# Kernel tuning notes

Measured on AMD Instinct MI355X. Metric: run time of the kernel, lower is better.

## Reference

```python
import math
import jax, jax.numpy as jnp
import numpy as np

R = 4  # upsample_factor
C_FEAT = 22
FEAT_SLICES = {4: (0, 9), 6: (9, 22)}
SH_SLICES = {0: (0, 1), 2: (1, 6)}
AGG_PATHS = [(4, 0, 4), (4, 2, 4), (4, 2, 6), (6, 0, 6), (6, 2, 4), (6, 2, 6)]
TP_PATHS = [(4, 4, 4), (4, 4, 6), (4, 6, 4), (4, 6, 6), (6, 4, 4), (6, 4, 6), (6, 6, 4), (6, 6, 6)]
AGG_NPATH = {4: 3, 6: 3}
TP_NPATH = {4: 4, 6: 4}


def _cg(j1, m1, j2, m2, j3, m3):
    # Condon-Shortley Clebsch-Gordan <j1 m1 j2 m2 | j3 m3> (Racah formula)
    if m1 + m2 != m3:
        return 0.0
    f = math.factorial
    pre = (2 * j3 + 1) * f(j1 + j2 - j3) * f(j1 - j2 + j3) * f(-j1 + j2 + j3) / f(j1 + j2 + j3 + 1)
    pre *= f(j1 + m1) * f(j1 - m1) * f(j2 + m2) * f(j2 - m2) * f(j3 + m3) * f(j3 - m3)
    kmin = max(0, j2 - j3 - m1, j1 - j3 + m2)
    kmax = min(j1 + j2 - j3, j1 - m1, j2 + m2)
    s = 0.0
    for k in range(kmin, kmax + 1):
        s += (-1) ** k / (f(k) * f(j1 + j2 - j3 - k) * f(j1 - m1 - k) * f(j2 + m2 - k) * f(j3 - j2 + m1 + k) * f(j3 - j1 - m2 + k))
    return math.sqrt(pre) * s


def _q(l):
    # change of basis real SH -> complex SH (rows: real m, cols: complex m), with (-i)^l phase
    q = np.zeros((2 * l + 1, 2 * l + 1), dtype=np.complex128)
    q[l, l] = 1.0
    s2 = 1.0 / math.sqrt(2.0)
    for m in range(1, l + 1):
        q[l + m, l + m] = (-1) ** m * s2
        q[l + m, l - m] = s2
        q[l - m, l - m] = 1j * s2
        q[l - m, l + m] = -1j * (-1) ** m * s2
    return ((-1j) ** l) * q


def _w3j_real(l1, l2, l3):
    # Wigner 3j tensor in the real spherical-harmonic basis (invariant, unit Frobenius norm)
    w = np.zeros((2 * l1 + 1, 2 * l2 + 1, 2 * l3 + 1))
    for m1 in range(-l1, l1 + 1):
        for m2 in range(-l2, l2 + 1):
            m3 = -(m1 + m2)
            if abs(m3) <= l3:
                w[l1 + m1, l2 + m2, l3 + m3] = ((-1) ** (l1 - l2 - m3)) / math.sqrt(2 * l3 + 1) * _cg(l1, m1, l2, m2, l3, -m3)
    c = np.einsum('ai,bj,ck,ijk->abc', _q(l1), _q(l2), _q(l3), w.astype(np.complex128))
    return np.real(c).astype(np.float32)  # l1+l2+l3 even -> real


CG = {p: jnp.asarray(_w3j_real(*p)) for p in set(AGG_PATHS) | set(TP_PATHS)}


def _sh_kernel():
    # even-l real SH (integral normalization) at the 4 fixed 2x2 kernel directions
    s = 1.0 / math.sqrt(2.0)
    dirs = np.array([[-s, -s, 0.0], [s, -s, 0.0], [-s, s, 0.0], [s, s, 0.0]])
    x, y, z = dirs[:, 0], dirs[:, 1], dirs[:, 2]
    c2 = math.sqrt(15.0 / math.pi)
    sh = np.stack([
        np.full(4, 0.5 / math.sqrt(math.pi)),      # l=0
        0.5 * c2 * x * y,                           # l=2, m=-2
        0.5 * c2 * y * z,                           # l=2, m=-1
        0.25 * math.sqrt(5.0 / math.pi) * (3 * z ** 2 - 1.0),  # l=2, m=0
        0.5 * c2 * x * z,                           # l=2, m=1
        0.25 * c2 * (x ** 2 - y ** 2),              # l=2, m=2
    ], axis=1)
    return jnp.asarray(sh.astype(np.float32))  # (4, 6)


SH_KERNEL = _sh_kernel()


def setup_inputs() -> dict:
    key = jax.random.key(0)
    k1, k2, k3, k4 = jax.random.split(key, 4)
    H = W = 256
    return {
        'f4': jax.random.normal(k1, (H * W, 9), dtype=jnp.float32),
        'f6': jax.random.normal(k2, (H * W, 13), dtype=jnp.float32),
        'img_h': H,
        'img_w': W,
        'w_agg': jax.random.normal(k3, (6,), dtype=jnp.float32) * 0.1,
        'w_tp': jax.random.normal(k4, (8,), dtype=jnp.float32) * 0.1,
    }


def reference(f4, f6, img_h, img_w, w_agg, w_tp):
    H, W = int(img_h), int(img_w)
    Hr, Wr = H * R, W * R
    N = Hr * Wr
    # 1. nearest-neighbour upsample of concatenated irreps (H,W,22) -> (Hr,Wr,22)
    feat = jnp.concatenate([f4, f6], axis=-1).reshape(H, W, C_FEAT)
    feat_hr = jnp.repeat(jnp.repeat(feat, R, axis=0), R, axis=1)
    # 2. gather 2x2 patches with replicate padding (matches unfold k ordering (dh,dw))
    pad = jnp.pad(feat_hr, ((0, 1), (0, 1), (0, 0)), mode='edge')
    patches = jnp.stack([pad[dh:dh + Hr, dw:dw + Wr] for dh, dw in ((0, 0), (0, 1), (1, 0), (1, 1))], axis=2)
    patches = patches.reshape(N, 4, C_FEAT)  # (N,4,22)
    # tp_aggregate(neighbour, sh) summed over the 4 neighbours -> context (N,22)
    context = jnp.zeros((N, C_FEAT), dtype=feat.dtype)
    for i, (l1, l2, l3) in enumerate(AGG_PATHS):
        a0, a1 = FEAT_SLICES[l1]
        b0, b1 = SH_SLICES[l2]
        c0, c1 = FEAT_SLICES[l3]
        alpha = math.sqrt((2 * l3 + 1) / AGG_NPATH[l3])
        contrib = jnp.einsum('nka,kb,abc->nc', patches[:, :, a0:a1], SH_KERNEL[:, b0:b1], CG[(l1, l2, l3)])
        context = context.at[:, c0:c1].add((w_agg[i] * alpha) * contrib)
    # 3. tp(feat_self, context)
    feat_flat = feat_hr.reshape(N, C_FEAT)
    out = jnp.zeros((N, C_FEAT), dtype=feat.dtype)
    for i, (l1, l2, l3) in enumerate(TP_PATHS):
        a0, a1 = FEAT_SLICES[l1]
        b0, b1 = FEAT_SLICES[l2]
        c0, c1 = FEAT_SLICES[l3]
        alpha = math.sqrt((2 * l3 + 1) / TP_NPATH[l3])
        contrib = jnp.einsum('na,nb,abc->nc', feat_flat[:, a0:a1], context[:, b0:b1], CG[(l1, l2, l3)])
        out = out.at[:, c0:c1].add((w_tp[i] * alpha) * contrib)
    # 4. residual from the NN-upsampled features
    f4_out = out[:, :9] + feat_flat[:, :9]
    f6_out = out[:, 9:] + feat_flat[:, 9:]
    return f4_out, f6_out, (Hr, Wr)
```

## Files before the change

kernel.cpp:

```cpp
#include <hip/hip_runtime.h>
#include <hip/hip_bf16.h>
#include <math.h>

typedef __attribute__((ext_vector_type(8))) short short8;
typedef __attribute__((ext_vector_type(4))) float f32x4;
typedef __attribute__((ext_vector_type(2))) float f32x2;

__constant__ float c_fact[20] = {
    1.0f, 1.0f, 2.0f, 6.0f, 24.0f, 120.0f, 720.0f, 5040.0f, 40320.0f, 362880.0f,
    3628800.0f, 39916800.0f, 479001600.0f, 6227020800.0f, 87178291200.0f,
    1307674368000.0f, 20922789888000.0f, 355687428096000.0f,
    6402373705728000.0f, 121645100408832000.0f};
__constant__ float c_invf[20] = {
    1.0f, 1.0f, 0.5f, 0.16666666666666666f, 0.041666666666666664f,
    0.008333333333333333f, 0.001388888888888889f, 1.984126984126984e-4f,
    2.48015873015873e-5f, 2.755731922398589e-6f, 2.755731922398589e-7f,
    2.505210838544172e-8f, 2.08767569878681e-9f, 1.6059043836821613e-10f,
    1.1470745597729725e-11f, 7.647163731819816e-13f, 4.779477332387385e-14f,
    2.8114572543455206e-15f, 1.5619206968586225e-16f, 8.22063524662433e-18f};

__device__ float cgd(int j1, int m1, int j2, int m2, int j3, int m3) {
  if (m1 + m2 != m3) return 0.0f;
  float pre = (float)(2 * j3 + 1) * c_fact[j1 + j2 - j3] * c_fact[j1 - j2 + j3] *
              c_fact[-j1 + j2 + j3] * c_invf[j1 + j2 + j3 + 1];
  pre *= c_fact[j1 + m1] * c_fact[j1 - m1] * c_fact[j2 + m2] * c_fact[j2 - m2] *
         c_fact[j3 + m3] * c_fact[j3 - m3];
  int kmin = max(0, max(j2 - j3 - m1, j1 - j3 + m2));
  int kmax = min(j1 + j2 - j3, min(j1 - m1, j2 + m2));
  float s = 0.0f;
  for (int k = kmin; k <= kmax; ++k) {
    float d = c_invf[k] * c_invf[j1 + j2 - j3 - k] * c_invf[j1 - m1 - k] *
              c_invf[j2 + m2 - k] * c_invf[j3 - j2 + m1 + k] * c_invf[j3 - j1 - m2 + k];
    s += ((k & 1) ? -d : d);
  }
  return sqrtf(pre) * s;
}

__device__ float wstd(int l1, int l2, int l3, int i, int j, int k) {
  int m1 = i - l1, m2 = j - l2, m3 = k - l3;
  if (m1 + m2 + m3 != 0) return 0.0f;
  int e = l1 - l2 - m3;
  float sgn = (e & 1) ? -1.0f : 1.0f;
  return sgn * (1.0f / sqrtf((float)(2 * l3 + 1))) * cgd(l1, m1, l2, m2, l3, -m3);
}

__device__ int qrow(int l, int a, int idx[2], float vr[2], float vi[2]) {
  const float s2 = 0.70710678118654752440f;
  int m = a - l;
  if (m == 0) { idx[0] = l; vr[0] = 1.0f; vi[0] = 0.0f; return 1; }
  if (m > 0) {
    idx[0] = l + m; vr[0] = (m & 1) ? -s2 : s2; vi[0] = 0.0f;
    idx[1] = l - m; vr[1] = s2;                 vi[1] = 0.0f;
    return 2;
  }
  int mm = -m;
  idx[0] = l - mm; vr[0] = 0.0f; vi[0] = s2;
  idx[1] = l + mm; vr[1] = 0.0f; vi[1] = (mm & 1) ? s2 : -s2;
  return 2;
}

__device__ float w3j_real(int l1, int l2, int l3, int a, int b, int c) {
  int i1[2], i2[2], i3[2];
  float r1[2], s1[2], r2[2], s2v[2], r3[2], s3[2];
  int n1 = qrow(l1, a, i1, r1, s1);
  int n2 = qrow(l2, b, i2, r2, s2v);
  int n3 = qrow(l3, c, i3, r3, s3);
  float re = 0.0f;
  for (int x = 0; x < n1; ++x)
    for (int y = 0; y < n2; ++y)
      for (int z = 0; z < n3; ++z) {
        float w = wstd(l1, l2, l3, i1[x], i2[y], i3[z]);
        if (w == 0.0f) continue;
        float pr = r1[x] * r2[y] - s1[x] * s2v[y];
        float pi = r1[x] * s2v[y] + s1[x] * r2[y];
        float qr = pr * r3[z] - pi * s3[z];
        re += qr * w;
      }
  int L = l1 + l2 + l3;
  return ((L & 3) == 0) ? re : -re;
}

__device__ float sh_val(int k, int col) {
  const float PI_ = 3.14159265358979323846f;
  float sgn = (k == 0 || k == 3) ? 1.0f : -1.0f;
  if (col == 0) return 0.5f / sqrtf(PI_);
  if (col == 1) return sgn * 0.25f * sqrtf(15.0f / PI_);
  if (col == 3) return -0.25f * sqrtf(5.0f / PI_);
  return 0.0f;
}

__device__ __forceinline__ unsigned short bf16u(float x) {
  __hip_bfloat16 h = __float2bfloat16(x);
  return __builtin_bit_cast(unsigned short, h);
}
__device__ __forceinline__ float b2f(unsigned short u) {
  unsigned int v = ((unsigned int)u) << 16;
  return __builtin_bit_cast(float, v);
}

__global__ void eq_setup(const float* __restrict__ w_agg, const float* __restrict__ w_tp,
                         const int* __restrict__ ph, const int* __restrict__ pw,
                         float* __restrict__ out, long long tail_off,
                         unsigned short* __restrict__ ws) {
  int gid = blockIdx.x * 256 + threadIdx.x;
  if (gid == 0) {
    out[tail_off]     = (float)(ph[0] * 4);
    out[tail_off + 1] = (float)(pw[0] * 4);
  }
  if (gid < 22528) {
    int a = gid >> 10;
    int rem = gid & 1023;
    int nt = rem >> 9;
    int l = (rem >> 3) & 63;
    int e = rem & 7;
    int b = ((l >> 4) << 3) + e;
    int c = nt * 16 + (l & 15);
    float v = 0.f;
    if (b < 22 && c < 22) {
      int l1 = (a < 9) ? 4 : 6, l2 = (b < 9) ? 4 : 6, l3 = (c < 9) ? 4 : 6;
      int a_ = (a < 9) ? a : a - 9, b_ = (b < 9) ? b : b - 9, c_ = (c < 9) ? c : c - 9;
      int idx = ((l1 == 6) ? 4 : 0) + ((l2 == 6) ? 2 : 0) + ((l3 == 6) ? 1 : 0);
      float alpha = sqrtf((float)(2 * l3 + 1) * 0.25f);
      v = w_tp[idx] * alpha * w3j_real(l1, l2, l3, a_, b_, c_);
    }
    int pk = __builtin_amdgcn_cvt_pk_fp8_f32(v, 0.f, 0, 0);
    ((unsigned char*)ws)[gid] = (unsigned char)(pk & 0xff);
  } else if (gid < 26624) {
    int s = gid - 22528;
    int km = s >> 10;
    int rem = s & 1023;
    int nt = rem >> 9;
    int l = (rem >> 3) & 63;
    int e = rem & 7;
    int a = ((l >> 4) << 3) + e;
    int c = nt * 16 + (l & 15);
    float v = 0.f;
    if (a < 22 && c < 22) {
      int l1 = (a < 9) ? 4 : 6, l3 = (c < 9) ? 4 : 6;
      int a_ = (a < 9) ? a : a - 9, c_ = (c < 9) ? c : c - 9;
      float acc = 0.0f;
      float alpha = sqrtf((float)(2 * l3 + 1) / 3.0f);
      if (l1 == l3) {
        int i = (l1 == 4) ? 0 : 3;
        acc += w_agg[i] * alpha * sh_val(km, 0) * w3j_real(l1, 0, l3, a_, 0, c_);
      }
      {
        int i = (l1 == 4) ? ((l3 == 4) ? 1 : 2) : ((l3 == 4) ? 4 : 5);
        float t = 0.0f;
        for (int bb = 0; bb < 5; ++bb) {
          float shv = sh_val(km, 1 + bb);
          if (shv != 0.0f) t += shv * w3j_real(l1, 2, l3, a_, bb, c_);
        }
        acc += w_agg[i] * alpha * t;
      }
      v = acc;
    }
    ws[11264 + s] = bf16u(v);
  }
}

__device__ __forceinline__ void load_lds16(const unsigned int* g, unsigned int* l) {
  __builtin_amdgcn_global_load_lds(
      (const __attribute__((address_space(1))) unsigned int*)g,
      (__attribute__((address_space(3))) unsigned int*)l, 16, 0, 0);
}

#define WAVE_LDS_FENCE() do { \
    asm volatile("s_waitcnt lgkmcnt(0)" ::: "memory"); \
    __builtin_amdgcn_sched_barrier(0); } while (0)

__global__ __launch_bounds__(512, 6) void eq_main(
    const float* __restrict__ f4, const float* __restrict__ f6,
    const int* __restrict__ ph, const int* __restrict__ pw,
    const unsigned short* __restrict__ ws, float* __restrict__ out) {
  const int H = ph[0], Wc = pw[0];
  const int bx = (Wc + 31) >> 5;
  const long long ntiles = (long long)bx * H;
  const int Wr = Wc << 2;
  const long long Npix = (long long)H * Wc * 16;
  float* out6 = out + Npix * 9;

  __shared__ __align__(16) unsigned short LDS[23040];

  const int tid = threadIdx.x;
  const int wv = tid >> 6;
  const int l = tid & 63;
  const long long t = blockIdx.x;
  if (t >= ntiles) return;

  const int y0 = (int)(t / bx);
  const int x0 = (int)(t - (long long)y0 * bx) << 5;
  const int cw0 = x0 + (wv << 2);
  const int SLOT = 11264 + wv * 1472;

  {
    const unsigned int* src = (const unsigned int*)ws;
    unsigned int* dst = (unsigned int*)LDS;
#pragma unroll
    for (int i = 0; i < 3; ++i) {
      int chunk = i * 8 + wv;
      if (chunk < 22) load_lds16(src + chunk * 256 + l * 4, dst + chunk * 256);
    }
  }

  short8 mb[8];
  {
    const unsigned short* msrc = ws + 11264;
#pragma unroll
    for (int i = 0; i < 8; ++i) mb[i] = *(const short8*)(msrc + i * 512 + l * 8);
  }

#pragma unroll
  for (int k = 0; k < 2; ++k) {
    int e = k * 64 + l;
    if (e < 110) {
      int px = e / 11, pr = e - px * 11;
      int dyR = px / 5, col = px - dyR * 5;
      int yy = min(y0 + dyR, H - 1);
      int xx = min(cw0 + col, Wc - 1);
      long long p = (long long)yy * Wc + xx;
      int ca = 2 * pr;
      float v0 = (ca < 9) ? f4[p * 9 + ca] : f6[p * 13 + ca - 9];
      float v1 = (ca + 1 < 9) ? f4[p * 9 + ca + 1] : f6[p * 13 + ca - 8];
      unsigned int pk = (unsigned int)bf16u(v0) | ((unsigned int)bf16u(v1) << 16);
      *(unsigned int*)&LDS[SLOT + px * 24 + ca] = pk;
    } else if (e < 120) {
      *(unsigned int*)&LDS[SLOT + (e - 110) * 24 + 22] = 0u;
    }
  }

  __syncthreads();

  const int l15 = l & 15;
  const int lg = l >> 4;
  const int q = l15 & 3;
  const int lcell = l15 >> 2;
  const int a0 = lg << 3;

  f32x4 c0 = {0.f, 0.f, 0.f, 0.f}, c1 = {0.f, 0.f, 0.f, 0.f};
#pragma unroll
  for (int km = 0; km < 4; ++km) {
    short8 av = (short8)0;
    if (a0 < 24) {
      int dy = (km >> 1) & (q >> 1);
      int dx = km & q & 1;
      av = *(const short8*)&LDS[SLOT + (dy * 5 + lcell + dx) * 24 + a0];
    }
    c0 = __builtin_amdgcn_mfma_f32_16x16x32_bf16(av, mb[2 * km], c0, 0, 0, 0);
    c1 = __builtin_amdgcn_mfma_f32_16x16x32_bf16(av, mb[2 * km + 1], c1, 0, 0, 0);
  }

  unsigned int fvp[11];
  {
    const unsigned int* fp = (const unsigned int*)&LDS[SLOT + lcell * 24];
#pragma unroll
    for (int j = 0; j < 11; ++j) fvp[j] = fp[j];
  }
  const float r4 = b2f(LDS[SLOT + lg * 24 + l15]);
  const float r6 = (l15 < 6) ? b2f(LDS[SLOT + lg * 24 + 16 + l15]) : 0.f;

  float* ctxf = (float*)&LDS[SLOT + 256];
#pragma unroll
  for (int r = 0; r < 4; ++r) {
    ctxf[l15 * 24 + (lg << 2) + r] = c0[r];
    int ch1 = 16 + (lg << 2) + r;
    if (ch1 < 22) ctxf[l15 * 24 + ch1] = c1[r];
  }
  if (lg == 0) { ctxf[l15 * 24 + 22] = 0.f; ctxf[l15 * 24 + 23] = 0.f; }
  WAVE_LDS_FENCE();

  f32x2 cv2[4];
  {
    f32x4 lo = {0.f, 0.f, 0.f, 0.f}, hi = {0.f, 0.f, 0.f, 0.f};
    if (a0 < 24) {
      lo = *(const f32x4*)(ctxf + l15 * 24 + a0);
      hi = *(const f32x4*)(ctxf + l15 * 24 + a0 + 4);
    }
    cv2[0][0] = lo[0]; cv2[0][1] = lo[1];
    cv2[1][0] = lo[2]; cv2[1][1] = lo[3];
    cv2[2][0] = hi[0]; cv2[2][1] = hi[1];
    cv2[3][0] = hi[2]; cv2[3][1] = hi[3];
  }
  WAVE_LDS_FENCE();

  f32x4 oE0 = {0.f, 0.f, 0.f, 0.f}, oE1 = {0.f, 0.f, 0.f, 0.f};
  f32x4 oO0 = {0.f, 0.f, 0.f, 0.f}, oO1 = {0.f, 0.f, 0.f, 0.f};
  const char* Wb = (const char*)LDS;
#pragma unroll
  for (int ap = 0; ap < 11; ++ap) {
    const float sE = __builtin_bit_cast(float, fvp[ap] << 16);
    const float sO = __builtin_bit_cast(float, fvp[ap] & 0xffff0000u);
    {
      const f32x2 s2 = {sE, sE};
      f32x2 p0 = cv2[0] * s2, p1 = cv2[1] * s2, p2 = cv2[2] * s2, p3 = cv2[3] * s2;
      int lo = __builtin_amdgcn_cvt_pk_fp8_f32(p0[0], p0[1], 0, 0);
      lo = __builtin_amdgcn_cvt_pk_fp8_f32(p1[0], p1[1], lo, 1);
      int hi = __builtin_amdgcn_cvt_pk_fp8_f32(p2[0], p2[1], 0, 0);
      hi = __builtin_amdgcn_cvt_pk_fp8_f32(p3[0], p3[1], hi, 1);
      long av = (long)(((unsigned long long)(unsigned int)hi << 32) | (unsigned int)lo);
      long w0 = *(const long*)(Wb + ap * 2048 + l * 8);
      long w1 = *(const long*)(Wb + ap * 2048 + 512 + l * 8);
      oE0 = __builtin_amdgcn_mfma_f32_16x16x32_fp8_fp8(av, w0, oE0, 0, 0, 0);
      oE1 = __builtin_amdgcn_mfma_f32_16x16x32_fp8_fp8(av, w1, oE1, 0, 0, 0);
    }
    {
      const f32x2 s2 = {sO, sO};
      f32x2 p0 = cv2[0] * s2, p1 = cv2[1] * s2, p2 = cv2[2] * s2, p3 = cv2[3] * s2;
      int lo = __builtin_amdgcn_cvt_pk_fp8_f32(p0[0], p0[1], 0, 0);
      lo = __builtin_amdgcn_cvt_pk_fp8_f32(p1[0], p1[1], lo, 1);
      int hi = __builtin_amdgcn_cvt_pk_fp8_f32(p2[0], p2[1], 0, 0);
      hi = __builtin_amdgcn_cvt_pk_fp8_f32(p3[0], p3[1], hi, 1);
      long av = (long)(((unsigned long long)(unsigned int)hi << 32) | (unsigned int)lo);
      long w0 = *(const long*)(Wb + ap * 2048 + 1024 + l * 8);
      long w1 = *(const long*)(Wb + ap * 2048 + 1536 + l * 8);
      oO0 = __builtin_amdgcn_mfma_f32_16x16x32_fp8_fp8(av, w0, oO0, 0, 0, 0);
      oO1 = __builtin_amdgcn_mfma_f32_16x16x32_fp8_fp8(av, w1, oO1, 0, 0, 0);
    }
  }

  float* px4 = (float*)&LDS[SLOT];
  float* px6 = px4 + 288;
#pragma unroll
  for (int r = 0; r < 4; ++r) {
    const float v  = oE0[r] + oO0[r] + r4;
    const float v1 = oE1[r] + oO1[r] + r6;
    const int qy = r >> 1;
    float* p4 = px4 + qy * 144;
    float* p6 = px6 + qy * 208;
    if (r & 1) {
      const int px = (lg << 2) + 3;
      if (l15 < 9) p4[px * 9 + l15] = v; else p6[px * 13 + l15 - 9] = v;
      if (l15 < 6) p6[px * 13 + 7 + l15] = v1;
    } else {
#pragma unroll
      for (int dx = 0; dx < 3; ++dx) {
        const int px = (lg << 2) + dx;
        if (l15 < 9) p4[px * 9 + l15] = v; else p6[px * 13 + l15 - 9] = v;
        if (l15 < 6) p6[px * 13 + 7 + l15] = v1;
      }
    }
  }
  WAVE_LDS_FENCE();

  const long long y4 = (long long)(y0 << 2);
  if (cw0 + 4 <= Wc) {
#pragma unroll
    for (int ry = 0; ry < 4; ++ry) {
      const int qy = (ry == 3) ? 1 : 0;
      float* o4p = out + ((y4 + ry) * Wr + (cw0 << 2)) * 9;
      float* o6p = out6 + ((y4 + ry) * Wr + (cw0 << 2)) * 13;
      if (l < 36) *(f32x4*)(o4p + (l << 2)) = *(const f32x4*)(px4 + qy * 144 + (l << 2));
      if (l < 52) *(f32x4*)(o6p + (l << 2)) = *(const f32x4*)(px6 + qy * 208 + (l << 2));
    }
  } else {
    const int px = l & 15;
    const int ry = l >> 4;
    const int qy = (ry == 3) ? 1 : 0;
    const int hrx = (cw0 << 2) + px;
    if (hrx < Wr) {
      const long long rowb = (y4 + ry) * Wr + hrx;
      float* o4 = out + rowb * 9;
      float* o6 = out6 + rowb * 13;
#pragma unroll
      for (int ch = 0; ch < 9; ++ch) o4[ch] = px4[qy * 144 + px * 9 + ch];
#pragma unroll
      for (int ch = 0; ch < 13; ++ch) o6[ch] = px6[qy * 208 + px * 13 + ch];
    }
  }
}

extern "C" void kernel_launch(void* const* d_in, const int* in_sizes, int n_in,
                              void* d_out, int out_size, void* d_ws, size_t ws_size,
                              hipStream_t stream) {
  const float* f4 = (const float*)d_in[0];
  const float* f6 = (const float*)d_in[1];
  const int* ph = (const int*)d_in[2];
  const int* pw = (const int*)d_in[3];
  const float* wagg = (const float*)d_in[4];
  const float* wtp = (const float*)d_in[5];
  float* out = (float*)d_out;
  unsigned short* wsu = (unsigned short*)d_ws;

  long long HW = (long long)in_sizes[0] / 9;
  long long tail = (long long)out_size - 2;

  eq_setup<<<104, 256, 0, stream>>>(wagg, wtp, ph, pw, out, tail, wsu);

  int S = (int)(sqrt((double)HW) + 0.5);
  long long nb;
  if ((long long)S * S == HW) {
    nb = (long long)((S + 31) / 32) * S;
  } else {
    nb = HW;
  }
  eq_main<<<(int)nb, 512, 0, stream>>>(f4, f6, ph, pw, wsu, out);
}
```

Before: 46.09 us.

## Interleave fp8 TP weights for 128-bit LDS loads and vectorize LDS traffic

Reorders the fp8 tensor-product weight table in the workspace so each lane's four 8-byte MFMA B operands sit next to each other, letting the inner loop fetch them with two 16-byte LDS reads instead of four 8-byte reads. The per-pixel feature read and the context write-back now use vector LDS accesses instead of scalar loops. The block-wide barrier after patch staging becomes a wave-local fence, and a block barrier is placed before the weight-consuming loop with a wave fence after it. This cuts LDS instruction count but depends on the new barrier placement still ordering the cooperative weight staging and the per-wave scratch reuse correctly.

Result: no change. 46.56 us (+1.0%).

```diff
diff --git a/kernel.cpp b/kernel.cpp
--- a/kernel.cpp
+++ b/kernel.cpp
@@ -5,6 +5,9 @@
 typedef __attribute__((ext_vector_type(8))) short short8;
 typedef __attribute__((ext_vector_type(4))) float f32x4;
 typedef __attribute__((ext_vector_type(2))) float f32x2;
+typedef __attribute__((ext_vector_type(4))) unsigned int u32x4;
+typedef __attribute__((ext_vector_type(2))) unsigned int u32x2;
+typedef __attribute__((ext_vector_type(2))) long long2v;
 
 __constant__ float c_fact[20] = {
     1.0f, 1.0f, 2.0f, 6.0f, 24.0f, 120.0f, 720.0f, 5040.0f, 40320.0f, 362880.0f,
@@ -124,7 +127,8 @@
       v = w_tp[idx] * alpha * w3j_real(l1, l2, l3, a_, b_, c_);
     }
     int pk = __builtin_amdgcn_cvt_pk_fp8_f32(v, 0.f, 0, 0);
-    ((unsigned char*)ws)[gid] = (unsigned char)(pk & 0xff);
+    int nidx = ((a >> 1) << 11) + l * 32 + ((((a & 1) << 1) | nt) << 3) + e;
+    ((unsigned char*)ws)[nidx] = (unsigned char)(pk & 0xff);
   } else if (gid < 26624) {
     int s = gid - 22528;
     int km = s >> 10;
@@ -228,8 +232,7 @@
       *(unsigned int*)&LDS[SLOT + (e - 110) * 24 + 22] = 0u;
     }
   }
-
-  __syncthreads();
+  WAVE_LDS_FENCE();
 
   const int l15 = l & 15;
   const int lg = l >> 4;
@@ -253,20 +256,27 @@
   unsigned int fvp[11];
   {
     const unsigned int* fp = (const unsigned int*)&LDS[SLOT + lcell * 24];
-#pragma unroll
-    for (int j = 0; j < 11; ++j) fvp[j] = fp[j];
+    u32x4 q0 = *(const u32x4*)fp;
+    u32x4 q1 = *(const u32x4*)(fp + 4);
+    u32x2 q2 = *(const u32x2*)(fp + 8);
+    unsigned int q3 = fp[10];
+#pragma unroll
+    for (int j = 0; j < 4; ++j) { fvp[j] = q0[j]; fvp[4 + j] = q1[j]; }
+    fvp[8] = q2[0]; fvp[9] = q2[1]; fvp[10] = q3;
   }
   const float r4 = b2f(LDS[SLOT + lg * 24 + l15]);
   const float r6 = (l15 < 6) ? b2f(LDS[SLOT + lg * 24 + 16 + l15]) : 0.f;
 
   float* ctxf = (float*)&LDS[SLOT + 256];
-#pragma unroll
-  for (int r = 0; r < 4; ++r) {
-    ctxf[l15 * 24 + (lg << 2) + r] = c0[r];
-    int ch1 = 16 + (lg << 2) + r;
-    if (ch1 < 22) ctxf[l15 * 24 + ch1] = c1[r];
-  }
-  if (lg == 0) { ctxf[l15 * 24 + 22] = 0.f; ctxf[l15 * 24 + 23] = 0.f; }
+  {
+    *(f32x4*)(ctxf + l15 * 24 + (lg << 2)) = c0;
+    if (lg == 0) {
+      *(f32x4*)(ctxf + l15 * 24 + 16) = c1;
+    } else if (lg == 1) {
+      f32x4 tail = {c1[0], c1[1], 0.f, 0.f};
+      *(f32x4*)(ctxf + l15 * 24 + 20) = tail;
+    }
+  }
   WAVE_LDS_FENCE();
 
   f32x2 cv2[4];
@@ -281,7 +291,8 @@
     cv2[2][0] = hi[0]; cv2[2][1] = hi[1];
     cv2[3][0] = hi[2]; cv2[3][1] = hi[3];
   }
-  WAVE_LDS_FENCE();
+
+  __syncthreads();
 
   f32x4 oE0 = {0.f, 0.f, 0.f, 0.f}, oE1 = {0.f, 0.f, 0.f, 0.f};
   f32x4 oO0 = {0.f, 0.f, 0.f, 0.f}, oO1 = {0.f, 0.f, 0.f, 0.f};
@@ -290,6 +301,8 @@
   for (int ap = 0; ap < 11; ++ap) {
     const float sE = __builtin_bit_cast(float, fvp[ap] << 16);
     const float sO = __builtin_bit_cast(float, fvp[ap] & 0xffff0000u);
+    const long2v wE = *(const long2v*)(Wb + ap * 2048 + l * 32);
+    const long2v wO = *(const long2v*)(Wb + ap * 2048 + l * 32 + 16);
     {
       const f32x2 s2 = {sE, sE};
       f32x2 p0 = cv2[0] * s2, p1 = cv2[1] * s2, p2 = cv2[2] * s2, p3 = cv2[3] * s2;
@@ -298,10 +311,8 @@
       int hi = __builtin_amdgcn_cvt_pk_fp8_f32(p2[0], p2[1], 0, 0);
       hi = __builtin_amdgcn_cvt_pk_fp8_f32(p3[0], p3[1], hi, 1);
       long av = (long)(((unsigned long long)(unsigned int)hi << 32) | (unsigned int)lo);
-      long w0 = *(const long*)(Wb + ap * 2048 + l * 8);
-      long w1 = *(const long*)(Wb + ap * 2048 + 512 + l * 8);
-      oE0 = __builtin_amdgcn_mfma_f32_16x16x32_fp8_fp8(av, w0, oE0, 0, 0, 0);
-      oE1 = __builtin_amdgcn_mfma_f32_16x16x32_fp8_fp8(av, w1, oE1, 0, 0, 0);
+      oE0 = __builtin_amdgcn_mfma_f32_16x16x32_fp8_fp8(av, wE[0], oE0, 0, 0, 0);
+      oE1 = __builtin_amdgcn_mfma_f32_16x16x32_fp8_fp8(av, wE[1], oE1, 0, 0, 0);
     }
     {
       const f32x2 s2 = {sO, sO};
@@ -311,12 +322,11 @@
       int hi = __builtin_amdgcn_cvt_pk_fp8_f32(p2[0], p2[1], 0, 0);
       hi = __builtin_amdgcn_cvt_pk_fp8_f32(p3[0], p3[1], hi, 1);
       long av = (long)(((unsigned long long)(unsigned int)hi << 32) | (unsigned int)lo);
-      long w0 = *(const long*)(Wb + ap * 2048 + 1024 + l * 8);
-      long w1 = *(const long*)(Wb + ap * 2048 + 1536 + l * 8);
-      oO0 = __builtin_amdgcn_mfma_f32_16x16x32_fp8_fp8(av, w0, oO0, 0, 0, 0);
-      oO1 = __builtin_amdgcn_mfma_f32_16x16x32_fp8_fp8(av, w1, oO1, 0, 0, 0);
-    }
-  }
+      oO0 = __builtin_amdgcn_mfma_f32_16x16x32_fp8_fp8(av, wO[0], oO0, 0, 0, 0);
+      oO1 = __builtin_amdgcn_mfma_f32_16x16x32_fp8_fp8(av, wO[1], oO1, 0, 0, 0);
+    }
+  }
+  WAVE_LDS_FENCE();
 
   float* px4 = (float*)&LDS[SLOT];
   float* px6 = px4 + 288;
```

## Process two tiles per block and share fp8 weight loads across both

Applied to the files above, without the earlier changes.

Each block now handles two consecutive tiles. Their inputs are staged into separate LDS slots, and both tiles' tensor-product MFMAs run in one loop. The fp8 weight table is re-laid out so each lane fetches its even and odd weight fragments with two 16-byte LDS reads, and those reads are reused for both tiles. This halves the block count and the per-tile cost of the weight staging and weight LDS reads. The price is more registers from doubled accumulators, which may cut occupancy, and a longer serial epilogue per block.

New measurement: 125.8 us. 2.73x slower.

```diff
diff --git a/kernel.cpp b/kernel.cpp
--- a/kernel.cpp
+++ b/kernel.cpp
@@ -5,6 +5,7 @@
 typedef __attribute__((ext_vector_type(8))) short short8;
 typedef __attribute__((ext_vector_type(4))) float f32x4;
 typedef __attribute__((ext_vector_type(2))) float f32x2;
+typedef __attribute__((ext_vector_type(2))) long long2v;
 
 __constant__ float c_fact[20] = {
     1.0f, 1.0f, 2.0f, 6.0f, 24.0f, 120.0f, 720.0f, 5040.0f, 40320.0f, 362880.0f,
@@ -124,7 +125,8 @@
       v = w_tp[idx] * alpha * w3j_real(l1, l2, l3, a_, b_, c_);
     }
     int pk = __builtin_amdgcn_cvt_pk_fp8_f32(v, 0.f, 0, 0);
-    ((unsigned char*)ws)[gid] = (unsigned char)(pk & 0xff);
+    int nidx = ((a >> 1) << 11) + l * 32 + ((((a & 1) << 1) | nt) << 3) + e;
+    ((unsigned char*)ws)[nidx] = (unsigned char)(pk & 0xff);
   } else if (gid < 26624) {
     int s = gid - 22528;
     int km = s >> 10;
@@ -180,18 +182,21 @@
   const long long Npix = (long long)H * Wc * 16;
   float* out6 = out + Npix * 9;
 
-  __shared__ __align__(16) unsigned short LDS[23040];
+  __shared__ __align__(16) unsigned short LDS[23552];
 
   const int tid = threadIdx.x;
   const int wv = tid >> 6;
   const int l = tid & 63;
-  const long long t = blockIdx.x;
-  if (t >= ntiles) return;
-
-  const int y0 = (int)(t / bx);
-  const int x0 = (int)(t - (long long)y0 * bx) << 5;
-  const int cw0 = x0 + (wv << 2);
-  const int SLOT = 11264 + wv * 1472;
+  const long long t0 = (long long)blockIdx.x * 2;
+  if (t0 >= ntiles) return;
+  const bool t1ok = (t0 + 1) < ntiles;
+  const long long t1e = t1ok ? (t0 + 1) : t0;
+
+  const int y0a = (int)(t0 / bx);
+  const int cw0a = (((int)(t0 - (long long)y0a * bx)) << 5) + (wv << 2);
+  const int y0b = (int)(t1e / bx);
+  const int cw0b = (((int)(t1e - (long long)y0b * bx)) << 5) + (wv << 2);
+  const int SLOT = 11264 + wv * 1536;
 
   {
     const unsigned int* src = (const unsigned int*)ws;
@@ -216,16 +221,28 @@
     if (e < 110) {
       int px = e / 11, pr = e - px * 11;
       int dyR = px / 5, col = px - dyR * 5;
-      int yy = min(y0 + dyR, H - 1);
-      int xx = min(cw0 + col, Wc - 1);
-      long long p = (long long)yy * Wc + xx;
       int ca = 2 * pr;
-      float v0 = (ca < 9) ? f4[p * 9 + ca] : f6[p * 13 + ca - 9];
-      float v1 = (ca + 1 < 9) ? f4[p * 9 + ca + 1] : f6[p * 13 + ca - 8];
-      unsigned int pk = (unsigned int)bf16u(v0) | ((unsigned int)bf16u(v1) << 16);
-      *(unsigned int*)&LDS[SLOT + px * 24 + ca] = pk;
+      {
+        int yy = min(y0a + dyR, H - 1);
+        int xx = min(cw0a + col, Wc - 1);
+        long long p = (long long)yy * Wc + xx;
+        float v0 = (ca < 9) ? f4[p * 9 + ca] : f6[p * 13 + ca - 9];
+        float v1 = (ca + 1 < 9) ? f4[p * 9 + ca + 1] : f6[p * 13 + ca - 8];
+        unsigned int pk = (unsigned int)bf16u(v0) | ((unsigned int)bf16u(v1) << 16);
+        *(unsigned int*)&LDS[SLOT + px * 24 + ca] = pk;
+      }
+      {
+        int yy = min(y0b + dyR, H - 1);
+        int xx = min(cw0b + col, Wc - 1);
+        long long p = (long long)yy * Wc + xx;
+        float v0 = (ca < 9) ? f4[p * 9 + ca] : f6[p * 13 + ca - 9];
+        float v1 = (ca + 1 < 9) ? f4[p * 9 + ca + 1] : f6[p * 13 + ca - 8];
+        unsigned int pk = (unsigned int)bf16u(v0) | ((unsigned int)bf16u(v1) << 16);
+        *(unsigned int*)&LDS[SLOT + 256 + px * 24 + ca] = pk;
+      }
     } else if (e < 120) {
       *(unsigned int*)&LDS[SLOT + (e - 110) * 24 + 22] = 0u;
+      *(unsigned int*)&LDS[SLOT + 256 + (e - 110) * 24 + 22] = 0u;
     }
   }
 
@@ -237,93 +254,169 @@
   const int lcell = l15 >> 2;
   const int a0 = lg << 3;
 
-  f32x4 c0 = {0.f, 0.f, 0.f, 0.f}, c1 = {0.f, 0.f, 0.f, 0.f};
-#pragma unroll
-  for (int km = 0; km < 4; ++km) {
-    short8 av = (short8)0;
-    if (a0 < 24) {
-      int dy = (km >> 1) & (q >> 1);
-      int dx = km & q & 1;
-      av = *(const short8*)&LDS[SLOT + (dy * 5 + lcell + dx) * 24 + a0];
-    }
-    c0 = __builtin_amdgcn_mfma_f32_16x16x32_bf16(av, mb[2 * km], c0, 0, 0, 0);
-    c1 = __builtin_amdgcn_mfma_f32_16x16x32_bf16(av, mb[2 * km + 1], c1, 0, 0, 0);
-  }
-
-  unsigned int fvp[11];
+  float* ctxf = (float*)&LDS[SLOT + 512];
+
+  unsigned int fvpa[11];
+  float r4a, r6a;
+  f32x2 cva[4];
   {
-    const unsigned int* fp = (const unsigned int*)&LDS[SLOT + lcell * 24];
-#pragma unroll
-    for (int j = 0; j < 11; ++j) fvp[j] = fp[j];
-  }
-  const float r4 = b2f(LDS[SLOT + lg * 24 + l15]);
-  const float r6 = (l15 < 6) ? b2f(LDS[SLOT + lg * 24 + 16 + l15]) : 0.f;
-
-  float* ctxf = (float*)&LDS[SLOT + 256];
-#pragma unroll
-  for (int r = 0; r < 4; ++r) {
-    ctxf[l15 * 24 + (lg << 2) + r] = c0[r];
-    int ch1 = 16 + (lg << 2) + r;
-    if (ch1 < 22) ctxf[l15 * 24 + ch1] = c1[r];
-  }
-  if (lg == 0) { ctxf[l15 * 24 + 22] = 0.f; ctxf[l15 * 24 + 23] = 0.f; }
+    f32x4 c0 = {0.f, 0.f, 0.f, 0.f}, c1 = {0.f, 0.f, 0.f, 0.f};
+#pragma unroll
+    for (int km = 0; km < 4; ++km) {
+      short8 av = (short8)0;
+      if (a0 < 24) {
+        int dy = (km >> 1) & (q >> 1);
+        int dx = km & q & 1;
+        av = *(const short8*)&LDS[SLOT + (dy * 5 + lcell + dx) * 24 + a0];
+      }
+      c0 = __builtin_amdgcn_mfma_f32_16x16x32_bf16(av, mb[2 * km], c0, 0, 0, 0);
+      c1 = __builtin_amdgcn_mfma_f32_16x16x32_bf16(av, mb[2 * km + 1], c1, 0, 0, 0);
+    }
+    {
+      const unsigned int* fp = (const unsigned int*)&LDS[SLOT + lcell * 24];
+#pragma unroll
+      for (int j = 0; j < 11; ++j) fvpa[j] = fp[j];
+    }
+    r4a = b2f(LDS[SLOT + lg * 24 + l15]);
+    r6a = (l15 < 6) ? b2f(LDS[SLOT + lg * 24 + 16 + l15]) : 0.f;
+#pragma unroll
+    for (int r = 0; r < 4; ++r) {
+      ctxf[l15 * 24 + (lg << 2) + r] = c0[r];
+      int ch1 = 16 + (lg << 2) + r;
+      if (ch1 < 22) ctxf[l15 * 24 + ch1] = c1[r];
+    }
+    if (lg == 0) { ctxf[l15 * 24 + 22] = 0.f; ctxf[l15 * 24 + 23] = 0.f; }
+    WAVE_LDS_FENCE();
+    {
+      f32x4 lo = {0.f, 0.f, 0.f, 0.f}, hi = {0.f, 0.f, 0.f, 0.f};
+      if (a0 < 24) {
+        lo = *(const f32x4*)(ctxf + l15 * 24 + a0);
+        hi = *(const f32x4*)(ctxf + l15 * 24 + a0 + 4);
+      }
+      cva[0][0] = lo[0]; cva[0][1] = lo[1];
+      cva[1][0] = lo[2]; cva[1][1] = lo[3];
+      cva[2][0] = hi[0]; cva[2][1] = hi[1];
+      cva[3][0] = hi[2]; cva[3][1] = hi[3];
+    }
+    WAVE_LDS_FENCE();
+  }
+
+  unsigned int fvpb[11];
+  float r4b, r6b;
+  f32x2 cvb[4];
+  {
+    f32x4 c0 = {0.f, 0.f, 0.f, 0.f}, c1 = {0.f, 0.f, 0.f, 0.f};
+#pragma unroll
+    for (int km = 0; km < 4; ++km) {
+      short8 av = (short8)0;
+      if (a0 < 24) {
+        int dy = (km >> 1) & (q >> 1);
+        int dx = km & q & 1;
+        av = *(const short8*)&LDS[SLOT + 256 + (dy * 5 + lcell + dx) * 24 + a0];
+      }
+      c0 = __builtin_amdgcn_mfma_f32_16x16x32_bf16(av, mb[2 * km], c0, 0, 0, 0);
+      c1 = __builtin_amdgcn_mfma_f32_16x16x32_bf16(av, mb[2 * km + 1], c1, 0, 0, 0);
+    }
+    {
+      const unsigned int* fp = (const unsigned int*)&LDS[SLOT + 256 + lcell * 24];
+#pragma unroll
+      for (int j = 0; j < 11; ++j) fvpb[j] = fp[j];
+    }
+    r4b = b2f(LDS[SLOT + 256 + lg * 24 + l15]);
+    r6b = (l15 < 6) ? b2f(LDS[SLOT + 256 + lg * 24 + 16 + l15]) : 0.f;
+#pragma unroll
+    for (int r = 0; r < 4; ++r) {
+      ctxf[l15 * 24 + (lg << 2) + r] = c0[r];
+      int ch1 = 16 + (lg << 2) + r;
+      if (ch1 < 22) ctxf[l15 * 24 + ch1] = c1[r];
+    }
+    if (lg == 0) { ctxf[l15 * 24 + 22] = 0.f; ctxf[l15 * 24 + 23] = 0.f; }
+    WAVE_LDS_FENCE();
+    {
+      f32x4 lo = {0.f, 0.f, 0.f, 0.f}, hi = {0.f, 0.f, 0.f, 0.f};
+      if (a0 < 24) {
+        lo = *(const f32x4*)(ctxf + l15 * 24 + a0);
+        hi = *(const f32x4*)(ctxf + l15 * 24 + a0 + 4);
+      }
+      cvb[0][0] = lo[0]; cvb[0][1] = lo[1];
+      cvb[1][0] = lo[2]; cvb[1][1] = lo[3];
+      cvb[2][0] = hi[0]; cvb[2][1] = hi[1];
+      cvb[3][0] = hi[2]; cvb[3][1] = hi[3];
+    }
+    WAVE_LDS_FENCE();
+  }
+
+  f32x4 aE0 = {0.f, 0.f, 0.f, 0.f}, aE1 = {0.f, 0.f, 0.f, 0.f};
+  f32x4 aO0 = {0.f, 0.f, 0.f, 0.f}, aO1 = {0.f, 0.f, 0.f, 0.f};
+  f32x4 bE0 = {0.f, 0.f, 0.f, 0.f}, bE1 = {0.f, 0.f, 0.f, 0.f};
+  f32x4 bO0 = {0.f, 0.f, 0.f, 0.f}, bO1 = {0.f, 0.f, 0.f, 0.f};
+  const char* Wb = (const char*)LDS;
+#pragma unroll
+  for (int ap = 0; ap < 11; ++ap) {
+    const long2v wE = *(const long2v*)(Wb + ap * 2048 + l * 32);
+    const long2v wO = *(const long2v*)(Wb + ap * 2048 + l * 32 + 16);
+    {
+      const float sE = __builtin_bit_cast(float, fvpa[ap] << 16);
+      const float sO = __builtin_bit_cast(float, fvpa[ap] & 0xffff0000u);
+      {
+        const f32x2 s2 = {sE, sE};
+        f32x2 p0 = cva[0] * s2, p1 = cva[1] * s2, p2 = cva[2] * s2, p3 = cva[3] * s2;
+        int lo = __builtin_amdgcn_cvt_pk_fp8_f32(p0[0], p0[1], 0, 0);
+        lo = __builtin_amdgcn_cvt_pk_fp8_f32(p1[0], p1[1], lo, 1);
+        int hi = __builtin_amdgcn_cvt_pk_fp8_f32(p2[0], p2[1], 0, 0);
+        hi = __builtin_amdgcn_cvt_pk_fp8_f32(p3[0], p3[1], hi, 1);
+        long av = (long)(((unsigned long long)(unsigned int)hi << 32) | (unsigned int)lo);
+        aE0 = __builtin_amdgcn_mfma_f32_16x16x32_fp8_fp8(av, wE[0], aE0, 0, 0, 0);
+        aE1 = __builtin_amdgcn_mfma_f32_16x16x32_fp8_fp8(av, wE[1], aE1, 0, 0, 0);
+      }
+      {
+        const f32x2 s2 = {sO, sO};
+        f32x2 p0 = cva[0] * s2, p1 = cva[1] * s2, p2 = cva[2] * s2, p3 = cva[3] * s2;
+        int lo = __builtin_amdgcn_cvt_pk_fp8_f32(p0[0], p0[1], 0, 0);
+        lo = __builtin_amdgcn_cvt_pk_fp8_f32(p1[0], p1[1], lo, 1);
+        int hi = __builtin_amdgcn_cvt_pk_fp8_f32(p2[0], p2[1], 0, 0);
+        hi = __builtin_amdgcn_cvt_pk_fp8_f32(p3[0], p3[1], hi, 1);
+        long av = (long)(((unsigned long long)(unsigned int)hi << 32) | (unsigned int)lo);
+        aO0 = __builtin_amdgcn_mfma_f32_16x16x32_fp8_fp8(av, wO[0], aO0, 0, 0, 0);
+        aO1 = __builtin_amdgcn_mfma_f32_16x16x32_fp8_fp8(av, wO[1], aO1, 0, 0, 0);
+      }
+    }
+    {
+      const float sE = __builtin_bit_cast(float, fvpb[ap] << 16);
+      const float sO = __builtin_bit_cast(float, fvpb[ap] & 0xffff0000u);
+      {
+        const f32x2 s2 = {sE, sE};
+        f32x2 p0 = cvb[0] * s2, p1 = cvb[1] * s2, p2 = cvb[2] * s2, p3 = cvb[3] * s2;
+        int lo = __builtin_amdgcn_cvt_pk_fp8_f32(p0[0], p0[1], 0, 0);
+        lo = __builtin_amdgcn_cvt_pk_fp8_f32(p1[0], p1[1], lo, 1);
+        int hi = __builtin_amdgcn_cvt_pk_fp8_f32(p2[0], p2[1], 0, 0);
+        hi = __builtin_amdgcn_cvt_pk_fp8_f32(p3[0], p3[1], hi, 1);
+        long av = (long)(((unsigned long long)(unsigned int)hi << 32) | (unsigned int)lo);
+        bE0 = __builtin_amdgcn_mfma_f32_16x16x32_fp8_fp8(av, wE[0], bE0, 0, 0, 0);
+        bE1 = __builtin_amdgcn_mfma_f32_16x16x32_fp8_fp8(av, wE[1], bE1, 0, 0, 0);
+      }
+      {
+        const f32x2 s2 = {sO, sO};
+        f32x2 p0 = cvb[0] * s2, p1 = cvb[1] * s2, p2 = cvb[2] * s2, p3 = cvb[3] * s2;
+        int lo = __builtin_amdgcn_cvt_pk_fp8_f32(p0[0], p0[1], 0, 0);
+        lo = __builtin_amdgcn_cvt_pk_fp8_f32(p1[0], p1[1], lo, 1);
+        int hi = __builtin_amdgcn_cvt_pk_fp8_f32(p2[0], p2[1], 0, 0);
+        hi = __builtin_amdgcn_cvt_pk_fp8_f32(p3[0], p3[1], hi, 1);
+        long av = (long)(((unsigned long long)(unsigned int)hi << 32) | (unsigned int)lo);
+        bO0 = __builtin_amdgcn_mfma_f32_16x16x32_fp8_fp8(av, wO[0], bO0, 0, 0, 0);
+        bO1 = __builtin_amdgcn_mfma_f32_16x16x32_fp8_fp8(av, wO[1], bO1, 0, 0, 0);
+      }
+    }
+  }
   WAVE_LDS_FENCE();
-
-  f32x2 cv2[4];
-  {
-    f32x4 lo = {0.f, 0.f, 0.f, 0.f}, hi = {0.f, 0.f, 0.f, 0.f};
-    if (a0 < 24) {
-      lo = *(const f32x4*)(ctxf + l15 * 24 + a0);
-      hi = *(const f32x4*)(ctxf + l15 * 24 + a0 + 4);
-    }
-    cv2[0][0] = lo[0]; cv2[0][1] = lo[1];
-    cv2[1][0] = lo[2]; cv2[1][1] = lo[3];
-    cv2[2][0] = hi[0]; cv2[2][1] = hi[1];
-    cv2[3][0] = hi[2]; cv2[3][1] = hi[3];
-  }
-  WAVE_LDS_FENCE();
-
-  f32x4 oE0 = {0.f, 0.f, 0.f, 0.f}, oE1 = {0.f, 0.f, 0.f, 0.f};
-  f32x4 oO0 = {0.f, 0.f, 0.f, 0.f}, oO1 = {0.f, 0.f, 0.f, 0.f};
-  const char* Wb = (const char*)LDS;
-#pragma unroll
-  for (int ap = 0; ap < 11; ++ap) {
-    const float sE = __builtin_bit_cast(float, fvp[ap] << 16);
-    const float sO = __builtin_bit_cast(float, fvp[ap] & 0xffff0000u);
-    {
-      const f32x2 s2 = {sE, sE};
-      f32x2 p0 = cv2[0] * s2, p1 = cv2[1] * s2, p2 = cv2[2] * s2, p3 = cv2[3] * s2;
-      int lo = __builtin_amdgcn_cvt_pk_fp8_f32(p0[0], p0[1], 0, 0);
-      lo = __builtin_amdgcn_cvt_pk_fp8_f32(p1[0], p1[1], lo, 1);
-      int hi = __builtin_amdgcn_cvt_pk_fp8_f32(p2[0], p2[1], 0, 0);
-      hi = __builtin_amdgcn_cvt_pk_fp8_f32(p3[0], p3[1], hi, 1);
-      long av = (long)(((unsigned long long)(unsigned int)hi << 32) | (unsigned int)lo);
-      long w0 = *(const long*)(Wb + ap * 2048 + l * 8);
-      long w1 = *(const long*)(Wb + ap * 2048 + 512 + l * 8);
-      oE0 = __builtin_amdgcn_mfma_f32_16x16x32_fp8_fp8(av, w0, oE0, 0, 0, 0);
-      oE1 = __builtin_amdgcn_mfma_f32_16x16x32_fp8_fp8(av, w1, oE1, 0, 0, 0);
-    }
-    {
-      const f32x2 s2 = {sO, sO};
-      f32x2 p0 = cv2[0] * s2, p1 = cv2[1] * s2, p2 = cv2[2] * s2, p3 = cv2[3] * s2;
-      int lo = __builtin_amdgcn_cvt_pk_fp8_f32(p0[0], p0[1], 0, 0);
-      lo = __builtin_amdgcn_cvt_pk_fp8_f32(p1[0], p1[1], lo, 1);
-      int hi = __builtin_amdgcn_cvt_pk_fp8_f32(p2[0], p2[1], 0, 0);
-      hi = __builtin_amdgcn_cvt_pk_fp8_f32(p3[0], p3[1], hi, 1);
-      long av = (long)(((unsigned long long)(unsigned int)hi << 32) | (unsigned int)lo);
-      long w0 = *(const long*)(Wb + ap * 2048 + 1024 + l * 8);
-      long w1 = *(const long*)(Wb + ap * 2048 + 1536 + l * 8);
-      oO0 = __builtin_amdgcn_mfma_f32_16x16x32_fp8_fp8(av, w0, oO0, 0, 0, 0);
-      oO1 = __builtin_amdgcn_mfma_f32_16x16x32_fp8_fp8(av, w1, oO1, 0, 0, 0);
-    }
-  }
 
   float* px4 = (float*)&LDS[SLOT];
   float* px6 = px4 + 288;
+
 #pragma unroll
   for (int r = 0; r < 4; ++r) {
-    const float v  = oE0[r] + oO0[r] + r4;
-    const float v1 = oE1[r] + oO1[r] + r6;
+    const float v  = aE0[r] + aO0[r] + r4a;
+    const float v1 = aE1[r] + aO1[r] + r6a;
     const int qy = r >> 1;
     float* p4 = px4 + qy * 144;
     float* p6 = px6 + qy * 208;
@@ -341,30 +434,81 @@
     }
   }
   WAVE_LDS_FENCE();
-
-  const long long y4 = (long long)(y0 << 2);
-  if (cw0 + 4 <= Wc) {
-#pragma unroll
-    for (int ry = 0; ry < 4; ++ry) {
+  {
+    const long long y4 = (long long)(y0a << 2);
+    if (cw0a + 4 <= Wc) {
+#pragma unroll
+      for (int ry = 0; ry < 4; ++ry) {
+        const int qy = (ry == 3) ? 1 : 0;
+        float* o4p = out + ((y4 + ry) * Wr + (cw0a << 2)) * 9;
+        float* o6p = out6 + ((y4 + ry) * Wr + (cw0a << 2)) * 13;
+        if (l < 36) *(f32x4*)(o4p + (l << 2)) = *(const f32x4*)(px4 + qy * 144 + (l << 2));
+        if (l < 52) *(f32x4*)(o6p + (l << 2)) = *(const f32x4*)(px6 + qy * 208 + (l << 2));
+      }
+    } else {
+      const int px = l & 15;
+      const int ry = l >> 4;
       const int qy = (ry == 3) ? 1 : 0;
-      float* o4p = out + ((y4 + ry) * Wr + (cw0 << 2)) * 9;
-      float* o6p = out6 + ((y4 + ry) * Wr + (cw0 << 2)) * 13;
-      if (l < 36) *(f32x4*)(o4p + (l << 2)) = *(const f32x4*)(px4 + qy * 144 + (l << 2));
-      if (l < 52) *(f32x4*)(o6p + (l << 2)) = *(const f32x4*)(px6 + qy * 208 + (l << 2));
-    }
-  } else {
-    const int px = l & 15;
-    const int ry = l >> 4;
-    const int qy = (ry == 3) ? 1 : 0;
-    const int hrx = (cw0 << 2) + px;
-    if (hrx < Wr) {
-      const long long rowb = (y4 + ry) * Wr + hrx;
-      float* o4 = out + rowb * 9;
-      float* o6 = out6 + rowb * 13;
-#pragma unroll
-      for (int ch = 0; ch < 9; ++ch) o4[ch] = px4[qy * 144 + px * 9 + ch];
-#pragma unroll
-      for (int ch = 0; ch < 13; ++ch) o6[ch] = px6[qy * 208 + px * 13 + ch];
+      const int hrx = (cw0a << 2) + px;
+      if (hrx < Wr) {
+        const long long rowb = (y4 + ry) * Wr + hrx;
+        float* o4 = out + rowb * 9;
+        float* o6 = out6 + rowb * 13;
+#pragma unroll
+        for (int ch = 0; ch < 9; ++ch) o4[ch] = px4[qy * 144 + px * 9 + ch];
+#pragma unroll
+        for (int ch = 0; ch < 13; ++ch) o6[ch] = px6[qy * 208 + px * 13 + ch];
+      }
+    }
+  }
+  WAVE_LDS_FENCE();
+
+  if (t1ok) {
+#pragma unroll
+    for (int r = 0; r < 4; ++r) {
+      const float v  = bE0[r] + bO0[r] + r4b;
+      const float v1 = bE1[r] + bO1[r] + r6b;
+      const int qy = r >> 1;
+      float* p4 = px4 + qy * 144;
+      float* p6 = px6 + qy * 208;
+      if (r & 1) {
+        const int px = (lg << 2) + 3;
+        if (l15 < 9) p4[px * 9 + l15] = v; else p6[px * 13 + l15 - 9] = v;
+        if (l15 < 6) p6[px * 13 + 7 + l15] = v1;
+      } else {
+#pragma unroll
+        for (int dx = 0; dx < 3; ++dx) {
+          const int px = (lg << 2) + dx;
+          if (l15 < 9) p4[px * 9 + l15] = v; else p6[px * 13 + l15 - 9] = v;
+          if (l15 < 6) p6[px * 13 + 7 + l15] = v1;
+        }
+      }
+    }
+    WAVE_LDS_FENCE();
+    const long long y4 = (long long)(y0b << 2);
+    if (cw0b + 4 <= Wc) {
+#pragma unroll
+      for (int ry = 0; ry < 4; ++ry) {
+        const int qy = (ry == 3) ? 1 : 0;
+        float* o4p = out + ((y4 + ry) * Wr + (cw0b << 2)) * 9;
+        float* o6p = out6 + ((y4 + ry) * Wr + (cw0b << 2)) * 13;
+        if (l < 36) *(f32x4*)(o4p + (l << 2)) = *(const f32x4*)(px4 + qy * 144 + (l << 2));
+        if (l < 52) *(f32x4*)(o6p + (l << 2)) = *(const f32x4*)(px6 + qy * 208 + (l << 2));
+      }
+    } else {
+      const int px = l & 15;
+      const int ry = l >> 4;
+      const int qy = (ry == 3) ? 1 : 0;
+      const int hrx = (cw0b << 2) + px;
+      if (hrx < Wr) {
+        const long long rowb = (y4 + ry) * Wr + hrx;
+        float* o4 = out + rowb * 9;
+        float* o6 = out6 + rowb * 13;
+#pragma unroll
+        for (int ch = 0; ch < 9; ++ch) o4[ch] = px4[qy * 144 + px * 9 + ch];
+#pragma unroll
+        for (int ch = 0; ch < 13; ++ch) o6[ch] = px6[qy * 208 + px * 13 + ch];
+      }
     }
   }
 }
@@ -389,9 +533,10 @@
   int S = (int)(sqrt((double)HW) + 0.5);
   long long nb;
   if ((long long)S * S == HW) {
-    nb = (long long)((S + 31) / 32) * S;
+    long long nt = (long long)((S + 31) / 32) * S;
+    nb = (nt + 1) / 2;
   } else {
-    nb = HW;
+    nb = HW / 2 + 2;
   }
   eq_main<<<(int)nb, 512, 0, stream>>>(f4, f6, ph, pw, wsu, out);
 }
```
